# Optimization experiments

Measured on AMD Instinct MI355X. Metric: run time of the kernel, lower is better.

## Reference

```python
import jax, jax.numpy as jnp
import numpy as np

DIM = 768
B, N = 16, 1024
EPS_LN = 1e-5

def _layernorm(x, gamma, beta):
    mu = jnp.mean(x, axis=-1, keepdims=True)
    var = jnp.mean((x - mu) ** 2, axis=-1, keepdims=True)
    return (x - mu) * jax.lax.rsqrt(var + EPS_LN) * gamma + beta

def _gelu(x):
    return jax.nn.gelu(x, approximate=False)

def setup_inputs() -> dict:
    key = jax.random.key(0)
    ks = jax.random.split(key, 10)
    d = DIM
    s1 = 1.0 / np.sqrt(2 * d)
    s = 1.0 / np.sqrt(d)
    return {
        "x": jax.random.normal(ks[0], (B, N, d), dtype=jnp.float32),
        "gamma": jnp.ones((d,), jnp.float32),
        "beta": jnp.zeros((d,), jnp.float32),
        "w1": jax.random.normal(ks[1], (2 * d, d), jnp.float32) * s1,
        "b1": jnp.zeros((d,), jnp.float32),
        "w2": jax.random.normal(ks[2], (d, d), jnp.float32) * s,
        "b2": jnp.zeros((d,), jnp.float32),
        "w3": jax.random.normal(ks[3], (d, d), jnp.float32) * s,
        "b3": jnp.zeros((d,), jnp.float32),
        "w4": jax.random.normal(ks[4], (d, d), jnp.float32) * s,
        "b4": jnp.zeros((d,), jnp.float32),
    }

def reference(x, gamma, beta, w1, b1, w2, b2, w3, b3, w4, b4):
    # x: [B, N, D]
    avg_x = jnp.mean(x, axis=1)                      # [B, D]
    A = avg_x[:, None, :] * jax.nn.sigmoid(_layernorm(x, gamma, beta))  # [B, N, D]
    # batched pairwise Euclidean distance among tokens (replaces python loop)
    sq = jnp.sum(A * A, axis=-1)                     # [B, N]
    d2 = sq[:, :, None] + sq[:, None, :] - 2.0 * jnp.einsum('bnd,bmd->bnm', A, A)
    dist = jnp.sqrt(jnp.clip(d2, 1e-12))             # [B, N, N]
    m = jnp.max(dist, axis=-1)                       # [B, N]
    m_x = x + m[..., None]                           # [B, N, D]
    cat = jnp.concatenate([A, m_x], axis=-1)         # [B, N, 2D]
    m1 = _gelu(cat @ w1 + b1)                        # layer1
    W = _gelu(m1 @ w2 + b2)                          # layer2
    Wdyn = x * W
    l3 = _gelu((m1 * Wdyn) @ w3 + b3)                # layer3
    out = _gelu((x * l3) @ w4 + b4)                  # layer4
    return out.astype(jnp.float32)
```

## Files before the change

kernel.cpp:

```cpp
#include <hip/hip_runtime.h>
#include <hip/hip_fp16.h>
#include <math.h>

#define DIM 768
#define NTOK 1024
#define NBATCH 16
#define BNR (NBATCH * NTOK)

typedef _Float16 f16x8 __attribute__((ext_vector_type(8)));
typedef float f32x4 __attribute__((ext_vector_type(4)));

__device__ __forceinline__ void gl2lds16(const void* g, void* l) {
    __builtin_amdgcn_global_load_lds(
        (const __attribute__((address_space(1))) void*)g,
        (__attribute__((address_space(3))) void*)l, 16, 0, 0);
}

__device__ __forceinline__ float gelu_fast(float z) {
    const float s = z * 0.70710678118654752f;
    const float ax = fabsf(s);
    const float t = __builtin_amdgcn_rcpf(1.0f + 0.3275911f * ax);
    const float poly = t * (0.254829592f + t * (-0.284496736f +
                       t * (1.421413741f + t * (-1.453152027f + t * 1.061405429f))));
    const float e = __expf(-ax * ax);
    float erfv = 1.0f - poly * e;
    erfv = copysignf(erfv, s);
    return 0.5f * z * (1.0f + erfv);
}

__device__ __forceinline__ float block_sum(float v, float* sbuf) {
    #pragma unroll
    for (int o = 32; o > 0; o >>= 1) v += __shfl_down(v, o, 64);
    const int lane = threadIdx.x & 63, w = threadIdx.x >> 6;
    if (lane == 0) sbuf[w] = v;
    __syncthreads();
    const float r = sbuf[0] + sbuf[1] + sbuf[2] + sbuf[3];
    __syncthreads();
    return r;
}

__global__ __launch_bounds__(256) void avg_kernel(const float* __restrict__ x,
                                                  float* __restrict__ avgx) {
    const int d = blockIdx.x * 256 + threadIdx.x;
    const int b = blockIdx.y;
    const int n0 = blockIdx.z * 128;
    const float* xp = x + (size_t)b * NTOK * DIM + (size_t)n0 * DIM + d;
    float s = 0.0f;
    for (int n = 0; n < 128; ++n) s += xp[(size_t)n * DIM];
    atomicAdd(&avgx[b * DIM + d], s * (1.0f / NTOK));
}

__global__ __launch_bounds__(256) void ln_sig_kernel(
    const float* __restrict__ x, const float* __restrict__ gamma,
    const float* __restrict__ beta, const float* __restrict__ avgx,
    __half* __restrict__ Ah, float* __restrict__ sq)
{
    __shared__ float sbuf[4];
    const int row = blockIdx.x;
    const int b = row >> 10;
    const int tid = threadIdx.x;
    const float* xr = x + (size_t)row * DIM;
    float v[3];
    #pragma unroll
    for (int i = 0; i < 3; ++i) v[i] = xr[tid + 256 * i];
    const float mu = block_sum(v[0] + v[1] + v[2], sbuf) * (1.0f / DIM);
    float ss = 0.0f;
    #pragma unroll
    for (int i = 0; i < 3; ++i) { const float d = v[i] - mu; ss += d * d; }
    const float var = block_sum(ss, sbuf) * (1.0f / DIM);
    const float rstd = rsqrtf(var + 1e-5f);
    const float* ag = avgx + b * DIM;
    float qs = 0.0f;
    #pragma unroll
    for (int i = 0; i < 3; ++i) {
        const int d = tid + 256 * i;
        const float ln = (v[i] - mu) * rstd * gamma[d] + beta[d];
        const float sg = 1.0f / (1.0f + expf(-ln));
        const float a = ag[d] * sg;
        const __half h = __float2half(a);
        const float ar = __half2float(h);
        Ah[(size_t)row * DIM + d] = h;
        qs += ar * ar;
    }
    const float tot = block_sum(qs, sbuf);
    if (tid == 0) sq[row] = tot;
}

__global__ __launch_bounds__(256) void wconv(const float* __restrict__ w,
                                             __half* __restrict__ wT, int K, int N)
{
    __shared__ float t[64][65];
    const int k0 = blockIdx.y * 64, n0 = blockIdx.x * 64;
    const int tid = threadIdx.x;
    const int r = tid >> 4, c4 = (tid & 15) * 4;
    #pragma unroll
    for (int p = 0; p < 4; ++p) {
        const int rr = p * 16 + r;
        const float4 v = *(const float4*)&w[(size_t)(k0 + rr) * N + n0 + c4];
        t[rr][c4] = v.x; t[rr][c4 + 1] = v.y; t[rr][c4 + 2] = v.z; t[rr][c4 + 3] = v.w;
    }
    __syncthreads();
    #pragma unroll
    for (int p = 0; p < 4; ++p) {
        const int nn = p * 16 + r;
        ushort4 pk;
        pk.x = __half_as_ushort(__float2half(t[c4 + 0][nn]));
        pk.y = __half_as_ushort(__float2half(t[c4 + 1][nn]));
        pk.z = __half_as_ushort(__float2half(t[c4 + 2][nn]));
        pk.w = __half_as_ushort(__float2half(t[c4 + 3][nn]));
        *(ushort4*)&wT[(size_t)(n0 + nn) * K + k0 + c4] = pk;
    }
}

__global__ __launch_bounds__(256) void xm_kernel(const float* __restrict__ x,
                                                 const float* __restrict__ m,
                                                 __half* __restrict__ xmH) {
    const int row = blockIdx.x;
    const float mv = m[row];
    #pragma unroll
    for (int i = 0; i < 3; ++i) {
        const int d = threadIdx.x + i * 256;
        xmH[(size_t)row * DIM + d] = __float2half(x[(size_t)row * DIM + d] + mv);
    }
}

template<int K, bool CAT, int EPI>
__global__ __launch_bounds__(256, 4) void gemm16(
    const __half* __restrict__ A0, const __half* __restrict__ A1,
    const __half* __restrict__ BT, const float* __restrict__ bias,
    const float* __restrict__ xin, const __half* __restrict__ m1h,
    __half* __restrict__ outH, float* __restrict__ outF)
{
    __shared__ _Float16 As[2][128 * 32];
    __shared__ _Float16 Bs[2][128 * 32];
    const int tid = threadIdx.x;
    const int w = tid >> 6, lane = tid & 63;
    const int wu = __builtin_amdgcn_readfirstlane(w);
    const int wr = w >> 1, wc = w & 1;
    const int R0 = blockIdx.x * 128, J0 = blockIdx.y * 128;
    constexpr int rs = CAT ? DIM : K;
    const int srow = lane >> 2;
    const int sk8 = (((lane & 3) ^ ((lane >> 3) & 3))) * 8;
    const int fx = ((lane >> 4) ^ ((lane >> 1) & 3)) * 8;
    constexpr int NT = K / 32;

    f32x4 acc[4][4];
    #pragma unroll
    for (int mt = 0; mt < 4; ++mt)
        #pragma unroll
        for (int nt = 0; nt < 4; ++nt) {
            f32x4 z = {0.0f, 0.0f, 0.0f, 0.0f};
            acc[mt][nt] = z;
        }

    auto stage = [&](int buf, int k0) {
        const __half* Ab = (CAT && k0 >= DIM) ? (A1 + (k0 - DIM)) : (A0 + k0);
        #pragma unroll
        for (int i = 0; i < 2; ++i) {
            const int rbase = i * 64 + w * 16;
            const int rbu = i * 64 + wu * 16;
            gl2lds16(Ab + (size_t)(R0 + rbase + srow) * rs + sk8, &As[buf][rbu * 32]);
            gl2lds16(BT + (size_t)(J0 + rbase + srow) * K + k0 + sk8, &Bs[buf][rbu * 32]);
        }
    };

    stage(0, 0);
    __syncthreads();
    #pragma unroll 2
    for (int kt = 0; kt < NT; ++kt) {
        const int cur = kt & 1;
        if (kt + 1 < NT) stage(cur ^ 1, (kt + 1) * 32);
        f16x8 af[4], bf[4];
        #pragma unroll
        for (int mt = 0; mt < 4; ++mt)
            af[mt] = *(const f16x8*)&As[cur][(wr * 64 + mt * 16 + (lane & 15)) * 32 + fx];
        #pragma unroll
        for (int nt = 0; nt < 4; ++nt)
            bf[nt] = *(const f16x8*)&Bs[cur][(wc * 64 + nt * 16 + (lane & 15)) * 32 + fx];
        #pragma unroll
        for (int mt = 0; mt < 4; ++mt)
            #pragma unroll
            for (int nt = 0; nt < 4; ++nt)
                acc[mt][nt] = __builtin_amdgcn_mfma_f32_16x16x32_f16(af[mt], bf[nt], acc[mt][nt], 0, 0, 0);
        __syncthreads();
    }

    #pragma unroll
    for (int mt = 0; mt < 4; ++mt) {
        #pragma unroll
        for (int nt = 0; nt < 4; ++nt) {
            const int col = J0 + wc * 64 + nt * 16 + (lane & 15);
            const float bv = bias[col];
            #pragma unroll
            for (int r = 0; r < 4; ++r) {
                const int row = R0 + wr * 64 + mt * 16 + (lane >> 4) * 4 + r;
                const size_t off = (size_t)row * DIM + col;
                const float g = gelu_fast(acc[mt][nt][r] + bv);
                if (EPI == 0) {
                    outH[off] = __float2half(g);
                } else if (EPI == 1) {
                    outH[off] = __float2half(__half2float(m1h[off]) * xin[off] * g);
                } else if (EPI == 2) {
                    outH[off] = __float2half(xin[off] * g);
                } else {
                    outF[off] = g;
                }
            }
        }
    }
}

__global__ __launch_bounds__(256, 4) void dist16(const __half* __restrict__ Ah,
                                                 const float* __restrict__ sq,
                                                 float* __restrict__ m)
{
    __shared__ _Float16 As[2][128 * 32];
    __shared__ _Float16 Bs[2][128 * 32];
    const int tid = threadIdx.x;
    const int w = tid >> 6, lane = tid & 63;
    const int wu = __builtin_amdgcn_readfirstlane(w);
    const int wr = w >> 1, wc = w & 1;
    const int base = blockIdx.x * NTOK;
    const int I0 = blockIdx.y * 128, J0 = blockIdx.z * 128;
    const int srow = lane >> 2;
    const int sk8 = (((lane & 3) ^ ((lane >> 3) & 3))) * 8;
    const int fx = ((lane >> 4) ^ ((lane >> 1) & 3)) * 8;
    constexpr int NT = DIM / 32;

    f32x4 acc[4][4];
    #pragma unroll
    for (int mt = 0; mt < 4; ++mt)
        #pragma unroll
        for (int nt = 0; nt < 4; ++nt) {
            f32x4 z = {0.0f, 0.0f, 0.0f, 0.0f};
            acc[mt][nt] = z;
        }

    auto stage = [&](int buf, int k0) {
        #pragma unroll
        for (int i = 0; i < 2; ++i) {
            const int rbase = i * 64 + w * 16;
            const int rbu = i * 64 + wu * 16;
            gl2lds16(Ah + (size_t)(base + I0 + rbase + srow) * DIM + k0 + sk8, &As[buf][rbu * 32]);
            gl2lds16(Ah + (size_t)(base + J0 + rbase + srow) * DIM + k0 + sk8, &Bs[buf][rbu * 32]);
        }
    };

    stage(0, 0);
    __syncthreads();
    #pragma unroll 2
    for (int kt = 0; kt < NT; ++kt) {
        const int cur = kt & 1;
        if (kt + 1 < NT) stage(cur ^ 1, (kt + 1) * 32);
        f16x8 af[4], bf[4];
        #pragma unroll
        for (int mt = 0; mt < 4; ++mt)
            af[mt] = *(const f16x8*)&As[cur][(wr * 64 + mt * 16 + (lane & 15)) * 32 + fx];
        #pragma unroll
        for (int nt = 0; nt < 4; ++nt)
            bf[nt] = *(const f16x8*)&Bs[cur][(wc * 64 + nt * 16 + (lane & 15)) * 32 + fx];
        #pragma unroll
        for (int mt = 0; mt < 4; ++mt)
            #pragma unroll
            for (int nt = 0; nt < 4; ++nt)
                acc[mt][nt] = __builtin_amdgcn_mfma_f32_16x16x32_f16(af[mt], bf[nt], acc[mt][nt], 0, 0, 0);
        __syncthreads();
    }

    #pragma unroll
    for (int mt = 0; mt < 4; ++mt) {
        float sqi[4];
        #pragma unroll
        for (int r = 0; r < 4; ++r)
            sqi[r] = sq[base + I0 + wr * 64 + mt * 16 + (lane >> 4) * 4 + r];
        float vmax[4] = {-1e30f, -1e30f, -1e30f, -1e30f};
        #pragma unroll
        for (int nt = 0; nt < 4; ++nt) {
            const float sqj = sq[base + J0 + wc * 64 + nt * 16 + (lane & 15)];
            #pragma unroll
            for (int r = 0; r < 4; ++r)
                vmax[r] = fmaxf(vmax[r], sqi[r] + sqj - 2.0f * acc[mt][nt][r]);
        }
        #pragma unroll
        for (int r = 0; r < 4; ++r) {
            float v = vmax[r];
            v = fmaxf(v, __shfl_xor(v, 1, 64));
            v = fmaxf(v, __shfl_xor(v, 2, 64));
            v = fmaxf(v, __shfl_xor(v, 4, 64));
            v = fmaxf(v, __shfl_xor(v, 8, 64));
            if ((lane & 15) == 0) {
                const float d = sqrtf(fmaxf(v, 1e-12f));
                atomicMax((unsigned int*)&m[base + I0 + wr * 64 + mt * 16 + (lane >> 4) * 4 + r],
                          __float_as_uint(d));
            }
        }
    }
}

extern "C" void kernel_launch(void* const* d_in, const int* in_sizes, int n_in,
                              void* d_out, int out_size, void* d_ws, size_t ws_size,
                              hipStream_t stream)
{
    const float* x     = (const float*)d_in[0];
    const float* gamma = (const float*)d_in[1];
    const float* beta  = (const float*)d_in[2];
    const float* w1    = (const float*)d_in[3];
    const float* b1    = (const float*)d_in[4];
    const float* w2    = (const float*)d_in[5];
    const float* b2    = (const float*)d_in[6];
    const float* w3    = (const float*)d_in[7];
    const float* b3    = (const float*)d_in[8];
    const float* w4    = (const float*)d_in[9];
    const float* b4    = (const float*)d_in[10];
    float* out = (float*)d_out;
    float* ws  = (float*)d_ws;

    float* avgx = ws;
    float* sq   = ws + 12288;
    float* mbuf = sq + 16384;
    __half* w1T = (__half*)(mbuf + 16384);
    __half* w2T = w1T + (size_t)1536 * 768;
    __half* w3T = w2T + (size_t)768 * 768;
    __half* w4T = w3T + (size_t)768 * 768;
    __half* P0  = w4T + (size_t)768 * 768;
    __half* P1  = P0 + (size_t)BNR * DIM;
    __half* Ah  = (__half*)d_out;
    __half* xmH = Ah + (size_t)BNR * DIM;

    hipMemsetAsync(avgx, 0, 12288 * sizeof(float), stream);
    hipMemsetAsync(mbuf, 0, BNR * sizeof(float), stream);
    wconv<<<dim3(12, 24), 256, 0, stream>>>(w1, w1T, 1536, 768);
    wconv<<<dim3(12, 12), 256, 0, stream>>>(w2, w2T, 768, 768);
    wconv<<<dim3(12, 12), 256, 0, stream>>>(w3, w3T, 768, 768);
    wconv<<<dim3(12, 12), 256, 0, stream>>>(w4, w4T, 768, 768);
    avg_kernel<<<dim3(3, NBATCH, 8), 256, 0, stream>>>(x, avgx);
    ln_sig_kernel<<<BNR, 256, 0, stream>>>(x, gamma, beta, avgx, Ah, sq);
    dist16<<<dim3(NBATCH, 8, 8), 256, 0, stream>>>(Ah, sq, mbuf);
    xm_kernel<<<BNR, 256, 0, stream>>>(x, mbuf, xmH);
    gemm16<1536, true, 0><<<dim3(128, 6), 256, 0, stream>>>(
        Ah, xmH, w1T, b1, nullptr, nullptr, P0, nullptr);
    gemm16<768, false, 1><<<dim3(128, 6), 256, 0, stream>>>(
        P0, nullptr, w2T, b2, x, P0, P1, nullptr);
    gemm16<768, false, 2><<<dim3(128, 6), 256, 0, stream>>>(
        P1, nullptr, w3T, b3, x, nullptr, P0, nullptr);
    gemm16<768, false, 3><<<dim3(128, 6), 256, 0, stream>>>(
        P0, nullptr, w4T, b4, x, nullptr, nullptr, out);
}
```

Measured before the change: 356.8 us.

## Exploit distance-matrix symmetry and merge weight-conversion launches and memsets

The pairwise distance kernel now launches only the 36 upper-triangular 128x128 tile pairs per batch instead of all 64. Each off-diagonal tile also reduces column maxima and atomically updates the max for the J rows, which roughly halves the Gram-matrix MFMA work. The three 768x768 weight conversions are fused into one launch using blockIdx.z. The workspace is reordered so avgx and mbuf sit next to each other and can be cleared with a single memset. The costs are a small loop that maps the linear tile index to (I, J), more atomics per tile, and extra register pressure from keeping the row and column squared norms in registers.

```diff
diff --git a/kernel.cpp b/kernel.cpp
--- a/kernel.cpp
+++ b/kernel.cpp
@@ -86,11 +86,12 @@
     if (tid == 0) sq[row] = tot;
 }
 
-__global__ __launch_bounds__(256) void wconv(const float* __restrict__ w,
-                                             __half* __restrict__ wT, int K, int N)
+__device__ __forceinline__ void wconv_body(const float* __restrict__ w,
+                                           __half* __restrict__ wT, int K, int N,
+                                           int bx, int by)
 {
     __shared__ float t[64][65];
-    const int k0 = blockIdx.y * 64, n0 = blockIdx.x * 64;
+    const int k0 = by * 64, n0 = bx * 64;
     const int tid = threadIdx.x;
     const int r = tid >> 4, c4 = (tid & 15) * 4;
     #pragma unroll
@@ -110,6 +111,24 @@
         pk.w = __half_as_ushort(__float2half(t[c4 + 3][nn]));
         *(ushort4*)&wT[(size_t)(n0 + nn) * K + k0 + c4] = pk;
     }
+}
+
+__global__ __launch_bounds__(256) void wconv(const float* __restrict__ w,
+                                             __half* __restrict__ wT, int K, int N)
+{
+    wconv_body(w, wT, K, N, blockIdx.x, blockIdx.y);
+}
+
+__global__ __launch_bounds__(256) void wconv3(const float* __restrict__ w2,
+                                              const float* __restrict__ w3,
+                                              const float* __restrict__ w4,
+                                              __half* __restrict__ t2,
+                                              __half* __restrict__ t3,
+                                              __half* __restrict__ t4)
+{
+    const float* w = (blockIdx.z == 0) ? w2 : (blockIdx.z == 1) ? w3 : w4;
+    __half* wT = (blockIdx.z == 0) ? t2 : (blockIdx.z == 1) ? t3 : t4;
+    wconv_body(w, wT, 768, 768, blockIdx.x, blockIdx.y);
 }
 
 __global__ __launch_bounds__(256) void xm_kernel(const float* __restrict__ x,
@@ -221,7 +240,10 @@
     const int wu = __builtin_amdgcn_readfirstlane(w);
     const int wr = w >> 1, wc = w & 1;
     const int base = blockIdx.x * NTOK;
-    const int I0 = blockIdx.y * 128, J0 = blockIdx.z * 128;
+    int t = blockIdx.y, ty = 0;
+    while (t >= 8 - ty) { t -= 8 - ty; ++ty; }
+    const int tz = ty + t;
+    const int I0 = ty * 128, J0 = tz * 128;
     const int srow = lane >> 2;
     const int sk8 = (((lane & 3) ^ ((lane >> 3) & 3))) * 8;
     const int fx = ((lane >> 4) ^ ((lane >> 1) & 3)) * 8;
@@ -267,20 +289,25 @@
         __syncthreads();
     }
 
+    float sqiA[4][4];
+    #pragma unroll
+    for (int mt = 0; mt < 4; ++mt)
+        #pragma unroll
+        for (int r = 0; r < 4; ++r)
+            sqiA[mt][r] = sq[base + I0 + wr * 64 + mt * 16 + (lane >> 4) * 4 + r];
+    float sqjA[4];
+    #pragma unroll
+    for (int nt = 0; nt < 4; ++nt)
+        sqjA[nt] = sq[base + J0 + wc * 64 + nt * 16 + (lane & 15)];
+
     #pragma unroll
     for (int mt = 0; mt < 4; ++mt) {
-        float sqi[4];
-        #pragma unroll
-        for (int r = 0; r < 4; ++r)
-            sqi[r] = sq[base + I0 + wr * 64 + mt * 16 + (lane >> 4) * 4 + r];
         float vmax[4] = {-1e30f, -1e30f, -1e30f, -1e30f};
         #pragma unroll
-        for (int nt = 0; nt < 4; ++nt) {
-            const float sqj = sq[base + J0 + wc * 64 + nt * 16 + (lane & 15)];
+        for (int nt = 0; nt < 4; ++nt)
             #pragma unroll
             for (int r = 0; r < 4; ++r)
-                vmax[r] = fmaxf(vmax[r], sqi[r] + sqj - 2.0f * acc[mt][nt][r]);
-        }
+                vmax[r] = fmaxf(vmax[r], sqiA[mt][r] + sqjA[nt] - 2.0f * acc[mt][nt][r]);
         #pragma unroll
         for (int r = 0; r < 4; ++r) {
             float v = vmax[r];
@@ -291,6 +318,25 @@
             if ((lane & 15) == 0) {
                 const float d = sqrtf(fmaxf(v, 1e-12f));
                 atomicMax((unsigned int*)&m[base + I0 + wr * 64 + mt * 16 + (lane >> 4) * 4 + r],
+                          __float_as_uint(d));
+            }
+        }
+    }
+
+    if (I0 != J0) {
+        #pragma unroll
+        for (int nt = 0; nt < 4; ++nt) {
+            float cm = -1e30f;
+            #pragma unroll
+            for (int mt = 0; mt < 4; ++mt)
+                #pragma unroll
+                for (int r = 0; r < 4; ++r)
+                    cm = fmaxf(cm, sqiA[mt][r] + sqjA[nt] - 2.0f * acc[mt][nt][r]);
+            cm = fmaxf(cm, __shfl_xor(cm, 16, 64));
+            cm = fmaxf(cm, __shfl_xor(cm, 32, 64));
+            if ((lane >> 4) == 0) {
+                const float d = sqrtf(fmaxf(cm, 1e-12f));
+                atomicMax((unsigned int*)&m[base + J0 + wc * 64 + nt * 16 + (lane & 15)],
                           __float_as_uint(d));
             }
         }
@@ -316,9 +362,9 @@
     float* ws  = (float*)d_ws;
 
     float* avgx = ws;
-    float* sq   = ws + 12288;
-    float* mbuf = sq + 16384;
-    __half* w1T = (__half*)(mbuf + 16384);
+    float* mbuf = ws + 12288;
+    float* sq   = mbuf + 16384;
+    __half* w1T = (__half*)(sq + 16384);
     __half* w2T = w1T + (size_t)1536 * 768;
     __half* w3T = w2T + (size_t)768 * 768;
     __half* w4T = w3T + (size_t)768 * 768;
@@ -327,15 +373,12 @@
     __half* Ah  = (__half*)d_out;
     __half* xmH = Ah + (size_t)BNR * DIM;
 
-    hipMemsetAsync(avgx, 0, 12288 * sizeof(float), stream);
-    hipMemsetAsync(mbuf, 0, BNR * sizeof(float), stream);
+    hipMemsetAsync(ws, 0, (12288 + 16384) * sizeof(float), stream);
     wconv<<<dim3(12, 24), 256, 0, stream>>>(w1, w1T, 1536, 768);
-    wconv<<<dim3(12, 12), 256, 0, stream>>>(w2, w2T, 768, 768);
-    wconv<<<dim3(12, 12), 256, 0, stream>>>(w3, w3T, 768, 768);
-    wconv<<<dim3(12, 12), 256, 0, stream>>>(w4, w4T, 768, 768);
+    wconv3<<<dim3(12, 12, 3), 256, 0, stream>>>(w2, w3, w4, w2T, w3T, w4T);
     avg_kernel<<<dim3(3, NBATCH, 8), 256, 0, stream>>>(x, avgx);
     ln_sig_kernel<<<BNR, 256, 0, stream>>>(x, gamma, beta, avgx, Ah, sq);
-    dist16<<<dim3(NBATCH, 8, 8), 256, 0, stream>>>(Ah, sq, mbuf);
+    dist16<<<dim3(NBATCH, 36), 256, 0, stream>>>(Ah, sq, mbuf);
     xm_kernel<<<BNR, 256, 0, stream>>>(x, mbuf, xmH);
     gemm16<1536, true, 0><<<dim3(128, 6), 256, 0, stream>>>(
         Ah, xmH, w1T, b1, nullptr, nullptr, P0, nullptr);
```

Result: faster. 334.2 us (-6.3%).
